# Kernel optimization log

Measured on AMD Instinct MI355X. Metric: run time of the kernel, lower is better.

Reference implementation:

```python
import jax, jax.numpy as jnp
import numpy as np

B, C_IN, C_OUT, H, W, W_DIM, K = 4, 64, 64, 512, 512, 512, 3
LRELU_SLOPE = 0.2
ACT_GAIN = np.sqrt(2.0).astype(np.float32)  # lrelu def_gain
CONV_CLAMP = 256.0


def setup_inputs() -> dict:
    key = jax.random.key(0)
    ks = jax.random.split(key, 5)
    return {
        "x": jax.random.normal(ks[0], (B, C_IN, H, W), dtype=jnp.float32),
        "ws": jax.random.normal(ks[1], (B, W_DIM), dtype=jnp.float32),
        "noise": jax.random.normal(ks[2], (B, 1, H, W), dtype=jnp.float32),
        "affine_weight": jax.random.normal(ks[3], (C_IN, W_DIM), dtype=jnp.float32),
        "affine_bias": jnp.ones((C_IN,), dtype=jnp.float32),
        "conv_weight": jax.random.normal(ks[4], (C_OUT, C_IN, K, K), dtype=jnp.float32),
        "bias": jnp.zeros((C_OUT,), dtype=jnp.float32),
    }


def reference(x, ws, noise, affine_weight, affine_bias, conv_weight, bias):
    b, c_in, h, w_sp = x.shape
    c_out, _, kh, kw = conv_weight.shape
    w_dim = ws.shape[1]

    # Affine (FullyConnectedLayer with equalized LR: weight_gain = 1/sqrt(w_dim), bias_init=1)
    styles = ws @ (affine_weight.T * np.float32(1.0 / np.sqrt(w_dim))) + affine_bias  # [b, c_in]

    # Modulate per-sample weights: w = weight[None] * styles
    wmod = conv_weight[None] * styles[:, None, :, None, None]  # [b, c_out, c_in, kh, kw]

    # Demodulation coefficients
    demod = jax.lax.rsqrt(jnp.sum(jnp.square(wmod), axis=(2, 3, 4)) + 1e-8)  # [b, c_out]
    wmod = wmod * demod[:, :, None, None, None]

    # Fused grouped conv: groups = batch (conv2d_resample, up=down=1, flip_weight=True -> correlation)
    xg = x.reshape(1, b * c_in, h, w_sp)
    wg = wmod.reshape(b * c_out, c_in, kh, kw)
    pad = kh // 2
    y = jax.lax.conv_general_dilated(
        xg, wg, window_strides=(1, 1), padding=[(pad, pad), (pad, pad)],
        dimension_numbers=("NCHW", "OIHW", "NCHW"), feature_group_count=b)
    y = y.reshape(b, c_out, h, w_sp)

    # Noise add (broadcast over channels)
    y = y + noise

    # bias_act: bias + lrelu * act_gain, then clamp (conv_clamp * gain, gain=1)
    y = y + bias[None, :, None, None]
    y = jnp.where(y >= 0, y, LRELU_SLOPE * y) * ACT_GAIN
    y = jnp.clip(y, -CONV_CLAMP, CONV_CLAMP)
    return y
```

## Files before the change

kernel.cpp:

```cpp
#include <hip/hip_runtime.h>
#include <math.h>

#define HH 512
#define WW 512
#define HW (HH * WW)
#define PW 514
#define PPIX (PW * PW)

#define A_U    36864
#define B_STR  12032
#define LDS_BYTES ((A_U + 2 * B_STR) * 2)

typedef short bf16x8 __attribute__((ext_vector_type(8)));
typedef float f32x4 __attribute__((ext_vector_type(4)));

__device__ __forceinline__ ushort f2bf(float f) {
    union { float f; uint u; } c; c.f = f;
    uint u = c.u;
    return (ushort)((u + 0x7fffu + ((u >> 16) & 1u)) >> 16);
}

__device__ __forceinline__ uint cvtpk(float a, float b) {
    uint r;
    asm("v_cvt_pk_bf16_f32 %0, %1, %2" : "=v"(r) : "v"(a), "v"(b));
    return r;
}

__global__ void k_styles(const float* __restrict__ wsv, const float* __restrict__ aw,
                         const float* __restrict__ ab, float* __restrict__ styles) {
    int bid = blockIdx.x;
    int b = bid >> 6, ci = bid & 63;
    int l = threadIdx.x;
    const float* wrow = wsv + b * 512;
    const float* arow = aw + ci * 512;
    float s = 0.f;
    #pragma unroll
    for (int j = 0; j < 8; ++j)
        s += wrow[l + 64 * j] * arow[l + 64 * j];
    #pragma unroll
    for (int off = 32; off; off >>= 1)
        s += __shfl_xor(s, off, 64);
    if (l == 0)
        styles[b * 64 + ci] = s * 0.044194173824159216f + ab[ci];
}

__global__ void k_wmod(const float* __restrict__ cw, const float* __restrict__ styles,
                       ushort* __restrict__ wb) {
    int b = blockIdx.x >> 6, co = blockIdx.x & 63;
    int ci = threadIdx.x;
    float st = styles[b * 64 + ci];
    const float* wp = cw + (co * 64 + ci) * 9;
    float wv[9];
    float ss = 0.f;
    #pragma unroll
    for (int k = 0; k < 9; ++k) { wv[k] = wp[k] * st; ss += wv[k] * wv[k]; }
    #pragma unroll
    for (int off = 32; off; off >>= 1)
        ss += __shfl_xor(ss, off, 64);
    float dm = 1.0f / sqrtf(ss + 1e-8f);
    int cisw = ((((ci >> 3) ^ co) & 7) << 3) | (ci & 7);
    #pragma unroll
    for (int k = 0; k < 9; ++k)
        wb[((size_t)(b * 64 + co) * 9 + k) * 64 + cisw] = f2bf(wv[k] * dm);
}

__global__ void k_zeropad(ushort* __restrict__ xp) {
    int id = blockIdx.x * 256 + threadIdx.x;
    if (id >= 4 * 2052) return;
    int b = id / 2052, r = id % 2052;
    int gyp, gxp;
    if (r < 514)       { gyp = 0;        gxp = r; }
    else if (r < 1028) { gyp = 513;      gxp = r - 514; }
    else if (r < 1540) { gyp = r - 1027; gxp = 0; }
    else               { gyp = r - 1539; gxp = 513; }
    ushort* p = xp + (((size_t)b * PW + gyp) * PW + gxp) * 64;
    uint4 z = make_uint4(0, 0, 0, 0);
    #pragma unroll
    for (int i = 0; i < 8; ++i) *(uint4*)(p + i * 8) = z;
}

__global__ __launch_bounds__(256) void k_xpose(
    const float* __restrict__ x, ushort* __restrict__ xp) {
    __shared__ ushort lt[128 * 68];
    const int t = threadIdx.x;
    const int bid = blockIdx.x;
    const int gxt = bid & 3;
    const int gy  = (bid >> 2) & 511;
    const int b   = bid >> 11;

    const float* xb = x + (size_t)b * 64 * HW + (size_t)gy * WW + gxt * 128;
    const int ci0 = 8 * (t >> 5);
    const int gxc = t & 31;

    f32x4 v[8];
    #pragma unroll
    for (int j = 0; j < 8; ++j)
        v[j] = *(const f32x4*)(xb + (size_t)(ci0 + j) * HW + gxc * 4);

    #pragma unroll
    for (int p = 0; p < 4; ++p) {
        int px = gxc * 4 + p;
        int rowp = ((px & 3) * 32 + (px >> 2)) * 68;
        #pragma unroll
        for (int cg = 0; cg < 2; ++cg) {
            uint lo = cvtpk(v[4 * cg + 0][p], v[4 * cg + 1][p]);
            uint hi = cvtpk(v[4 * cg + 2][p], v[4 * cg + 3][p]);
            *(uint2*)&lt[rowp + ci0 + 4 * cg] = make_uint2(lo, hi);
        }
    }
    __syncthreads();

    const int px = t >> 1, half = t & 1;
    const int rowp = ((px & 3) * 32 + (px >> 2)) * 68 + half * 32;
    uint4 o0 = *(uint4*)&lt[rowp + 0];
    uint4 o1 = *(uint4*)&lt[rowp + 8];
    uint4 o2 = *(uint4*)&lt[rowp + 16];
    uint4 o3 = *(uint4*)&lt[rowp + 24];
    ushort* dst = xp + (((size_t)b * PW + (gy + 1)) * PW + (gxt * 128 + px + 1)) * 64
                     + half * 32;
    *(uint4*)(dst + 0)  = o0;
    *(uint4*)(dst + 8)  = o1;
    *(uint4*)(dst + 16) = o2;
    *(uint4*)(dst + 24) = o3;
}

__device__ __forceinline__ void stage_b(ushort* lds, const ushort* __restrict__ xpb,
                                        int p, int tidx, int w, int lane) {
    const int ty = (tidx >> 5) * 8;
    const int tx = (tidx & 31) * 16;
    for (int j = w; j < 23; j += 4) {
        int c = j * 64 + lane;
        int c2 = c < 1439 ? c : 1439;
        int cig = c2 & 7;
        int pxl = c2 >> 3;
        int row = pxl / 18;
        int lcol = pxl - row * 18;
        int gsrc = cig ^ (lcol & 7);
        const ushort* src = xpb + ((size_t)(ty + row) * PW + (tx + lcol)) * 64 + gsrc * 8;
        __builtin_amdgcn_global_load_lds(
            (const __attribute__((address_space(1))) unsigned int*)src,
            (__attribute__((address_space(3))) unsigned int*)&lds[A_U + p * B_STR + j * 512],
            16, 0, 0);
    }
}

__global__ __launch_bounds__(256) void k_conv(
    const ushort* __restrict__ xp,
    const ushort* __restrict__ wb,
    const float* __restrict__ noise,
    const float* __restrict__ bias,
    float* __restrict__ out) {
    extern __shared__ __align__(16) ushort lds[];

    const int t = threadIdx.x;
    const int w = t >> 6;
    const int lane = t & 63;
    const int blk = blockIdx.x;
    const int b = blk >> 7;
    const int tile0 = (blk & 127) * 16;

    const ushort* xpb = xp + (size_t)b * PPIX * 64;
    const ushort* wA  = wb + (size_t)b * 64 * 576;

    for (int j = w; j < 72; j += 4) {
        const ushort* src = wA + j * 512 + lane * 8;
        __builtin_amdgcn_global_load_lds(
            (const __attribute__((address_space(1))) unsigned int*)src,
            (__attribute__((address_space(3))) unsigned int*)&lds[j * 512],
            16, 0, 0);
    }
    stage_b(lds, xpb, 0, tile0, w, lane);
    asm volatile("s_waitcnt vmcnt(0)" ::: "memory");
    __syncthreads();

    const int lr = lane & 15;
    const int lq = lane >> 4;

    int aidx[4][2];
    #pragma unroll
    for (int m = 0; m < 4; ++m)
        #pragma unroll
        for (int kb = 0; kb < 2; ++kb)
            aidx[m][kb] = (m * 16 + lr) * 576 + ((((kb << 2) | lq) ^ (lr & 7)) << 3);

    int bidx[2][3];
    #pragma unroll
    for (int i = 0; i < 2; ++i)
        #pragma unroll
        for (int dx = 0; dx < 3; ++dx) {
            int lcol = lr + dx;
            bidx[i][dx] = ((2 * w + i) * 18 + lcol) * 64 + ((lq * 8) ^ ((lcol & 7) << 3));
        }

    f32x4 bv[4];
    #pragma unroll
    for (int m = 0; m < 4; ++m)
        bv[m] = *(const f32x4*)&bias[m * 16 + lq * 4];
    const float* nz = noise + (size_t)b * HW;

    int p = 0;
    for (int it = 0; it < 16; ++it) {
        const int tidx = tile0 + it;
        const int ty = (tidx >> 5) * 8;
        const int tx = (tidx & 31) * 16;
        const int gx = tx + lr;

        if (it < 15) stage_b(lds, xpb, p ^ 1, tidx + 1, w, lane);

        float nv[2];
        int gyv[2];
        #pragma unroll
        for (int i = 0; i < 2; ++i) {
            gyv[i] = ty + 2 * w + i;
            nv[i] = nz[gyv[i] * WW + gx];
        }

        const ushort* bufp = &lds[A_U + p * B_STR];
        f32x4 acc[4][2];
        #pragma unroll
        for (int m = 0; m < 4; ++m)
            #pragma unroll
            for (int i = 0; i < 2; ++i) acc[m][i] = (f32x4){0.f, 0.f, 0.f, 0.f};

        #pragma unroll
        for (int dy = 0; dy < 3; ++dy) {
            #pragma unroll
            for (int dx = 0; dx < 3; ++dx) {
                #pragma unroll
                for (int kb = 0; kb < 2; ++kb) {
                    const int off = dy * 3 + dx;
                    bf16x8 afr[4], bfr[2];
                    #pragma unroll
                    for (int m = 0; m < 4; ++m)
                        afr[m] = *(const bf16x8*)&lds[aidx[m][kb] + off * 64];
                    #pragma unroll
                    for (int i = 0; i < 2; ++i) {
                        int idx = (bidx[i][dx] + dy * (18 * 64)) ^ (kb << 5);
                        bfr[i] = *(const bf16x8*)&bufp[idx];
                    }
                    #pragma unroll
                    for (int m = 0; m < 4; ++m)
                        #pragma unroll
                        for (int i = 0; i < 2; ++i)
                            acc[m][i] = __builtin_amdgcn_mfma_f32_16x16x32_bf16(
                                afr[m], bfr[i], acc[m][i], 0, 0, 0);
                }
            }
        }

        asm volatile("s_waitcnt vmcnt(0)" ::: "memory");
        __syncthreads();

        #pragma unroll
        for (int m = 0; m < 4; ++m) {
            #pragma unroll
            for (int i = 0; i < 2; ++i) {
                #pragma unroll
                for (int rg2 = 0; rg2 < 4; ++rg2) {
                    int co = m * 16 + lq * 4 + rg2;
                    float y = acc[m][i][rg2] + nv[i] + bv[m][rg2];
                    y = (y >= 0.f ? y : 0.2f * y) * 1.41421356237f;
                    y = fminf(fmaxf(y, -256.f), 256.f);
                    out[((size_t)(b * 64 + co) * HH + gyv[i]) * WW + gx] = y;
                }
            }
        }
        p ^= 1;
    }
}

extern "C" void kernel_launch(void* const* d_in, const int* in_sizes, int n_in,
                              void* d_out, int out_size, void* d_ws, size_t ws_size,
                              hipStream_t stream) {
    const float* x     = (const float*)d_in[0];
    const float* wsv   = (const float*)d_in[1];
    const float* noise = (const float*)d_in[2];
    const float* aw    = (const float*)d_in[3];
    const float* ab    = (const float*)d_in[4];
    const float* cw    = (const float*)d_in[5];
    const float* bias  = (const float*)d_in[6];
    float* out = (float*)d_out;

    float*  styles = (float*)d_ws;
    ushort* wb16   = (ushort*)((char*)d_ws + 1024);
    ushort* xpad   = (ushort*)((char*)d_ws + (1 << 20));

    hipFuncSetAttribute((const void*)k_conv,
                        hipFuncAttributeMaxDynamicSharedMemorySize, LDS_BYTES);

    k_styles<<<256, 64, 0, stream>>>(wsv, aw, ab, styles);
    k_wmod<<<256, 64, 0, stream>>>(cw, styles, wb16);
    k_zeropad<<<33, 256, 0, stream>>>(xpad);
    k_xpose<<<8192, 256, 0, stream>>>(x, xpad);
    k_conv<<<512, 256, LDS_BYTES, stream>>>(xpad, wb16, noise, bias, out);
}
```

Measured before the change: 267.5 us.

## Split conv output across eight waves per block and fold zero-padding into transpose

The conv kernel now launches 256 blocks of 512 threads instead of 512 blocks of 256. Each block walks a full 8-row band of 32 tiles, and its eight waves split the work 2x4 over output-channel groups and pixel rows. Each wave holds half as many accumulators and A fragments, which lowers register pressure and doubles the waves per CU available to hide LDS and global latency, at the cost of more B-fragment LDS reads relative to MFMA work. Separately, the border zero-padding kernel is merged into the transpose kernel as extra blocks, removing one launch.

```diff
diff --git a/kernel.cpp b/kernel.cpp
--- a/kernel.cpp
+++ b/kernel.cpp
@@ -7,9 +7,9 @@
 #define PW 514
 #define PPIX (PW * PW)
 
-#define A_U    36864
-#define B_STR  12032
-#define LDS_BYTES ((A_U + 2 * B_STR) * 2)
+#define A_U 36864
+#define B_U 11776
+#define LDS_BYTES ((A_U + 2 * B_U) * 2)
 
 typedef short bf16x8 __attribute__((ext_vector_type(8)));
 typedef float f32x4 __attribute__((ext_vector_type(4)));
@@ -64,26 +64,28 @@
         wb[((size_t)(b * 64 + co) * 9 + k) * 64 + cisw] = f2bf(wv[k] * dm);
 }
 
-__global__ void k_zeropad(ushort* __restrict__ xp) {
-    int id = blockIdx.x * 256 + threadIdx.x;
-    if (id >= 4 * 2052) return;
-    int b = id / 2052, r = id % 2052;
-    int gyp, gxp;
-    if (r < 514)       { gyp = 0;        gxp = r; }
-    else if (r < 1028) { gyp = 513;      gxp = r - 514; }
-    else if (r < 1540) { gyp = r - 1027; gxp = 0; }
-    else               { gyp = r - 1539; gxp = 513; }
-    ushort* p = xp + (((size_t)b * PW + gyp) * PW + gxp) * 64;
-    uint4 z = make_uint4(0, 0, 0, 0);
-    #pragma unroll
-    for (int i = 0; i < 8; ++i) *(uint4*)(p + i * 8) = z;
-}
-
 __global__ __launch_bounds__(256) void k_xpose(
     const float* __restrict__ x, ushort* __restrict__ xp) {
-    __shared__ ushort lt[128 * 68];
     const int t = threadIdx.x;
     const int bid = blockIdx.x;
+
+    if (bid >= 8192) {
+        int id = (bid - 8192) * 256 + t;
+        if (id >= 4 * 2052) return;
+        int b = id / 2052, r = id % 2052;
+        int gyp, gxp;
+        if (r < 514)       { gyp = 0;        gxp = r; }
+        else if (r < 1028) { gyp = 513;      gxp = r - 514; }
+        else if (r < 1540) { gyp = r - 1027; gxp = 0; }
+        else               { gyp = r - 1539; gxp = 513; }
+        ushort* p = xp + (((size_t)b * PW + gyp) * PW + gxp) * 64;
+        uint4 z = make_uint4(0, 0, 0, 0);
+        #pragma unroll
+        for (int i = 0; i < 8; ++i) *(uint4*)(p + i * 8) = z;
+        return;
+    }
+
+    __shared__ ushort lt[128 * 68];
     const int gxt = bid & 3;
     const int gy  = (bid >> 2) & 511;
     const int b   = bid >> 11;
@@ -125,10 +127,10 @@
 }
 
 __device__ __forceinline__ void stage_b(ushort* lds, const ushort* __restrict__ xpb,
-                                        int p, int tidx, int w, int lane) {
-    const int ty = (tidx >> 5) * 8;
-    const int tx = (tidx & 31) * 16;
-    for (int j = w; j < 23; j += 4) {
+                                        int p, int band, int ct, int w, int lane) {
+    const int ty = band * 8;
+    const int tx = ct * 16;
+    for (int j = w; j < 23; j += 8) {
         int c = j * 64 + lane;
         int c2 = c < 1439 ? c : 1439;
         int cig = c2 & 7;
@@ -139,12 +141,12 @@
         const ushort* src = xpb + ((size_t)(ty + row) * PW + (tx + lcol)) * 64 + gsrc * 8;
         __builtin_amdgcn_global_load_lds(
             (const __attribute__((address_space(1))) unsigned int*)src,
-            (__attribute__((address_space(3))) unsigned int*)&lds[A_U + p * B_STR + j * 512],
+            (__attribute__((address_space(3))) unsigned int*)&lds[A_U + p * B_U + j * 512],
             16, 0, 0);
     }
 }
 
-__global__ __launch_bounds__(256) void k_conv(
+__global__ __launch_bounds__(512) void k_conv(
     const ushort* __restrict__ xp,
     const ushort* __restrict__ wb,
     const float* __restrict__ noise,
@@ -156,32 +158,34 @@
     const int w = t >> 6;
     const int lane = t & 63;
     const int blk = blockIdx.x;
-    const int b = blk >> 7;
-    const int tile0 = (blk & 127) * 16;
+    const int b = blk >> 6;
+    const int band = blk & 63;
 
     const ushort* xpb = xp + (size_t)b * PPIX * 64;
     const ushort* wA  = wb + (size_t)b * 64 * 576;
 
-    for (int j = w; j < 72; j += 4) {
+    for (int j = w; j < 72; j += 8) {
         const ushort* src = wA + j * 512 + lane * 8;
         __builtin_amdgcn_global_load_lds(
             (const __attribute__((address_space(1))) unsigned int*)src,
             (__attribute__((address_space(3))) unsigned int*)&lds[j * 512],
             16, 0, 0);
     }
-    stage_b(lds, xpb, 0, tile0, w, lane);
+    stage_b(lds, xpb, 0, band, 0, w, lane);
     asm volatile("s_waitcnt vmcnt(0)" ::: "memory");
     __syncthreads();
 
     const int lr = lane & 15;
     const int lq = lane >> 4;
-
-    int aidx[4][2];
-    #pragma unroll
-    for (int m = 0; m < 4; ++m)
+    const int wm = w >> 2;
+    const int wn = w & 3;
+
+    int aidx[2][2];
+    #pragma unroll
+    for (int m = 0; m < 2; ++m)
         #pragma unroll
         for (int kb = 0; kb < 2; ++kb)
-            aidx[m][kb] = (m * 16 + lr) * 576 + ((((kb << 2) | lq) ^ (lr & 7)) << 3);
+            aidx[m][kb] = ((2 * wm + m) * 16 + lr) * 576 + ((((kb << 2) | lq) ^ (lr & 7)) << 3);
 
     int bidx[2][3];
     #pragma unroll
@@ -189,36 +193,35 @@
         #pragma unroll
         for (int dx = 0; dx < 3; ++dx) {
             int lcol = lr + dx;
-            bidx[i][dx] = ((2 * w + i) * 18 + lcol) * 64 + ((lq * 8) ^ ((lcol & 7) << 3));
-        }
-
-    f32x4 bv[4];
-    #pragma unroll
-    for (int m = 0; m < 4; ++m)
-        bv[m] = *(const f32x4*)&bias[m * 16 + lq * 4];
+            bidx[i][dx] = ((2 * wn + i) * 18 + lcol) * 64 + ((lq * 8) ^ ((lcol & 7) << 3));
+        }
+
+    f32x4 bv[2];
+    #pragma unroll
+    for (int m = 0; m < 2; ++m)
+        bv[m] = *(const f32x4*)&bias[(2 * wm + m) * 16 + lq * 4];
     const float* nz = noise + (size_t)b * HW;
+    const int ty = band * 8;
 
     int p = 0;
-    for (int it = 0; it < 16; ++it) {
-        const int tidx = tile0 + it;
-        const int ty = (tidx >> 5) * 8;
-        const int tx = (tidx & 31) * 16;
+    for (int it = 0; it < 32; ++it) {
+        const int tx = it * 16;
         const int gx = tx + lr;
 
-        if (it < 15) stage_b(lds, xpb, p ^ 1, tidx + 1, w, lane);
+        if (it < 31) stage_b(lds, xpb, p ^ 1, band, it + 1, w, lane);
 
         float nv[2];
         int gyv[2];
         #pragma unroll
         for (int i = 0; i < 2; ++i) {
-            gyv[i] = ty + 2 * w + i;
+            gyv[i] = ty + 2 * wn + i;
             nv[i] = nz[gyv[i] * WW + gx];
         }
 
-        const ushort* bufp = &lds[A_U + p * B_STR];
-        f32x4 acc[4][2];
-        #pragma unroll
-        for (int m = 0; m < 4; ++m)
+        const ushort* bufp = &lds[A_U + p * B_U];
+        f32x4 acc[2][2];
+        #pragma unroll
+        for (int m = 0; m < 2; ++m)
             #pragma unroll
             for (int i = 0; i < 2; ++i) acc[m][i] = (f32x4){0.f, 0.f, 0.f, 0.f};
 
@@ -229,9 +232,9 @@
                 #pragma unroll
                 for (int kb = 0; kb < 2; ++kb) {
                     const int off = dy * 3 + dx;
-                    bf16x8 afr[4], bfr[2];
+                    bf16x8 afr[2], bfr[2];
                     #pragma unroll
-                    for (int m = 0; m < 4; ++m)
+                    for (int m = 0; m < 2; ++m)
                         afr[m] = *(const bf16x8*)&lds[aidx[m][kb] + off * 64];
                     #pragma unroll
                     for (int i = 0; i < 2; ++i) {
@@ -239,7 +242,7 @@
                         bfr[i] = *(const bf16x8*)&bufp[idx];
                     }
                     #pragma unroll
-                    for (int m = 0; m < 4; ++m)
+                    for (int m = 0; m < 2; ++m)
                         #pragma unroll
                         for (int i = 0; i < 2; ++i)
                             acc[m][i] = __builtin_amdgcn_mfma_f32_16x16x32_bf16(
@@ -252,12 +255,12 @@
         __syncthreads();
 
         #pragma unroll
-        for (int m = 0; m < 4; ++m) {
+        for (int m = 0; m < 2; ++m) {
             #pragma unroll
             for (int i = 0; i < 2; ++i) {
                 #pragma unroll
                 for (int rg2 = 0; rg2 < 4; ++rg2) {
-                    int co = m * 16 + lq * 4 + rg2;
+                    int co = (2 * wm + m) * 16 + lq * 4 + rg2;
                     float y = acc[m][i][rg2] + nv[i] + bv[m][rg2];
                     y = (y >= 0.f ? y : 0.2f * y) * 1.41421356237f;
                     y = fminf(fmaxf(y, -256.f), 256.f);
@@ -290,7 +293,6 @@
 
     k_styles<<<256, 64, 0, stream>>>(wsv, aw, ab, styles);
     k_wmod<<<256, 64, 0, stream>>>(cw, styles, wb16);
-    k_zeropad<<<33, 256, 0, stream>>>(xpad);
-    k_xpose<<<8192, 256, 0, stream>>>(x, xpad);
-    k_conv<<<512, 256, LDS_BYTES, stream>>>(xpad, wb16, noise, bias, out);
-}
+    k_xpose<<<8225, 256, 0, stream>>>(x, xpad);
+    k_conv<<<256, 512, LDS_BYTES, stream>>>(xpad, wb16, noise, bias, out);
+}
```

New measurement: 253.5 us. 5.2% less time.
